# Performance work log

Hardware: AMD Instinct MI355X
Metric: run time of the kernel (lower is better)

## Reference

```python
import jax, jax.numpy as jnp
import numpy as np

HEADDIM = 128
CHUNK = 256


def _ssd_scan(x, dt, A, B, C, chunk):
    # x: (b,l,h,p)  dt: (b,l,h)  A: (h,)  B,C: (b,l,n)  (single group g=1 shared by all heads)
    b, l, h, p = x.shape
    n = B.shape[-1]
    nc = l // chunk
    dA = dt * A  # (b,l,h)
    xc = x.reshape(b, nc, chunk, h, p)
    dtc = dt.reshape(b, nc, chunk, h)
    dAc = dA.reshape(b, nc, chunk, h)
    Bc = B.reshape(b, nc, chunk, n)
    Cc = C.reshape(b, nc, chunk, n)
    cs = jnp.cumsum(dAc, axis=2)  # (b,nc,c,h) cumulative log-decay within chunk
    # intra-chunk quadratic part
    CB = jnp.einsum('bjin,bjkn->bjik', Cc, Bc)  # (b,nc,c,c)
    decay = jnp.exp(cs[:, :, :, None, :] - cs[:, :, None, :, :])  # (b,nc,i,k,h)
    mask = jnp.tril(jnp.ones((chunk, chunk), dtype=bool))
    decay = jnp.where(mask[None, None, :, :, None], decay, 0.0)
    y_intra = jnp.einsum('bjik,bjikh,bjkh,bjkhp->bjihp', CB, decay, dtc, xc)
    # per-chunk end states
    decay_states = jnp.exp(cs[:, :, -1:, :] - cs)  # (b,nc,c,h)
    states = jnp.einsum('bjkh,bjkh,bjkn,bjkhp->bjhnp', decay_states, dtc, Bc, xc)
    # recurrence across chunks: h_j = exp(sum dA_j) * h_{j-1} + states_j
    chunk_decay = jnp.exp(cs[:, :, -1, :])  # (b,nc,h)
    def step(carry, inp):
        s, d = inp
        new = carry * d[:, :, None, None] + s
        return new, carry  # emit state BEFORE this chunk
    init = jnp.zeros((b, h, n, p), x.dtype)
    _, prev = jax.lax.scan(step, init,
                           (states.transpose(1, 0, 2, 3, 4), chunk_decay.transpose(1, 0, 2)))
    prev = prev.transpose(1, 0, 2, 3, 4)  # (b,nc,h,n,p)
    y_inter = jnp.einsum('bjih,bjin,bjhnp->bjihp', jnp.exp(cs), Cc, prev)
    return (y_intra + y_inter).reshape(b, l, h, p)


def setup_inputs() -> dict:
    key = jax.random.key(0)
    k1, k2, k3, k4 = jax.random.split(key, 4)
    b, l, d_inner, nheads, d_state = 2, 4096, 2048, 16, 256
    x = jax.random.normal(k1, (b, l, d_inner), dtype=jnp.float32)
    BC = jax.random.normal(k2, (b, l, 2 * d_state), dtype=jnp.float32) * 0.1
    dt = jax.random.normal(k3, (b, l, 2 * nheads), dtype=jnp.float32) - 3.0
    A_log = jnp.zeros((nheads,), dtype=jnp.float32)
    D = jnp.ones((nheads,), dtype=jnp.float32)
    W_fcD = jax.random.normal(k4, (nheads, d_inner), dtype=jnp.float32) * 0.02
    return {"x": x, "BC": BC, "dt": dt, "A_log": A_log, "D": D, "W_fcD": W_fcD}


def reference(x, BC, dt, A_log, D, W_fcD):
    b, l, dim = x.shape
    h = A_log.shape[0]
    p = HEADDIM
    d_state = BC.shape[-1] // 2
    A = -jnp.exp(A_log)
    # bidirectional: concat forward stream with time-flipped backward stream along batch
    dt2 = jnp.concatenate((dt[:, :, :h], jnp.flip(dt[:, :, h:], axis=1)), axis=0)
    dt2 = jax.nn.softplus(dt2)
    x_og = x
    x2 = jnp.concatenate((x, jnp.flip(x, axis=1)), axis=0)
    BC2 = jnp.concatenate((BC, jnp.flip(BC, axis=1)), axis=0)
    B, C = BC2[..., :d_state], BC2[..., d_state:]
    y = _ssd_scan(x2.reshape(2 * b, l, h, p), dt2, A, B, C, CHUNK)
    y = y.reshape(2 * b, l, dim)
    y = jnp.roll(y, shift=1, axis=1).at[:, 0, :].set(0.0)
    y_fw, y_bw = y[:b], jnp.flip(y[b:], axis=1)
    gate = x_og @ W_fcD.T + D  # (b,l,h)
    y = y_fw + y_bw + x_og * jnp.repeat(gate, p, axis=-1)
    return y
```

## Files before the change

### kernel.cpp

```cpp
#include <hip/hip_runtime.h>
#include <stdint.h>

#define NB 2
#define SL 4096
#define NH 16
#define HD 128
#define DS 256
#define CK 256
#define NCH 16
#define NSQ 4
#define DI 2048

typedef unsigned short u16;
typedef unsigned int u32;
typedef __attribute__((ext_vector_type(8))) __bf16 bf16x8;
typedef __attribute__((ext_vector_type(4))) float f32x4;

__device__ __forceinline__ int tor(int dir, int t) { return dir ? (SL - 1 - t) : t; }

__device__ __forceinline__ u16 f2bf(float f) {
  u32 u = __float_as_uint(f);
  u = u + 0x7fffu + ((u >> 16) & 1u);
  return (u16)(u >> 16);
}
__device__ __forceinline__ float bf2f(u16 s) {
  return __uint_as_float(((u32)s) << 16);
}

__device__ __forceinline__ void gl_lds16(const u16* g, u16* l) {
  __builtin_amdgcn_global_load_lds((const __attribute__((address_space(1))) u32*)g,
                                   (__attribute__((address_space(3))) u32*)l, 16, 0, 0);
}

__device__ __forceinline__ void stage_tile(const u16* __restrict__ src, u16* lds,
                                           int lane, int w, int k0) {
  int sgrow = lane >> 2, sc = lane & 3;
  int r0 = w << 5;
  int ra = r0 + sgrow, rb = ra + 16;
  int kqa = (sc ^ ((ra >> 1) & 3)) << 3;
  int kqb = (sc ^ ((rb >> 1) & 3)) << 3;
  gl_lds16(src + (size_t)ra * 256 + k0 + kqa, lds + r0 * 32);
  gl_lds16(src + (size_t)rb * 256 + k0 + kqb, lds + (r0 + 16) * 32);
}

__device__ __forceinline__ bf16x8 frag(const u16* lds, int base_row, int m, int quad) {
  int row = base_row + m;
  return *(const bf16x8*)&lds[row * 32 + ((quad ^ ((row >> 1) & 3)) << 3)];
}

__device__ __forceinline__ void mfma16(const u16* As, const u16* Bs, int wi, int wp,
                                       int m, int quad, f32x4 acc[4][4]) {
  bf16x8 af[4], bv[4];
#pragma unroll
  for (int r = 0; r < 4; ++r) af[r] = frag(As, wi + (r << 4), m, quad);
#pragma unroll
  for (int c = 0; c < 4; ++c) bv[c] = frag(Bs, wp + (c << 4), m, quad);
#pragma unroll
  for (int r = 0; r < 4; ++r)
#pragma unroll
    for (int c = 0; c < 4; ++c)
      acc[r][c] = __builtin_amdgcn_mfma_f32_16x16x32_bf16(af[r], bv[c], acc[r][c], 0, 0, 0);
}

__global__ __launch_bounds__(256) void kprep(const float* __restrict__ dt,
                                             const float* __restrict__ A_log,
                                             float* __restrict__ csb,
                                             float* __restrict__ dtvb,
                                             float* __restrict__ cdecb) {
  int blk = blockIdx.x;
  int h = blk & 15, sj = blk >> 4;
  int s = sj >> 4, j = sj & 15;
  int b = s & 1, dir = s >> 1;
  int i = threadIdx.x;
  int to = tor(dir, j * CK + i);
  __shared__ float sbuf[CK];
  float a = -expf(A_log[h]);
  float raw = dt[((size_t)(b * SL + to)) * (2 * NH) + dir * NH + h];
  float sp = (raw > 20.f) ? raw : log1pf(expf(raw));
  sbuf[i] = sp * a;
  __syncthreads();
  for (int off = 1; off < CK; off <<= 1) {
    float v = (i >= off) ? sbuf[i - off] : 0.f;
    __syncthreads();
    sbuf[i] += v;
    __syncthreads();
  }
  float csv = sbuf[i];
  size_t base = ((size_t)sj * NH + h) * CK;
  csb[base + i] = csv;
  dtvb[base + i] = sp;
  if (i == CK - 1) cdecb[sj * NH + h] = expf(csv);
}

__global__ __launch_bounds__(256) void kcast(const float* __restrict__ BC,
                                             u16* __restrict__ Bbf,
                                             u16* __restrict__ Cbf) {
  int blk = blockIdx.x;
  int s = blk >> 12, t = blk & (SL - 1);
  int b = s & 1, dir = s >> 1;
  int tsrc = tor(dir, t);
  int tid = threadIdx.x;
  const float* src = BC + ((size_t)(b * SL + tsrc)) * (2 * DS);
  size_t dstb = ((size_t)s * SL + t) * DS;
  Bbf[dstb + tid] = f2bf(src[tid]);
  Cbf[dstb + tid] = f2bf(src[DS + tid]);
}

__global__ __launch_bounds__(256) void ktransB(const u16* __restrict__ Bbf,
                                               u16* __restrict__ BbfT) {
  int sj = blockIdx.x;
  int s = sj >> 4, j = sj & 15;
  __shared__ u16 T[64 * 264];
  int tid = threadIdx.x;
  const u16* src = Bbf + ((size_t)s * SL + j * CK) * DS;
  u16* dst = BbfT + (size_t)sj * DS * CK;
  int kr = tid >> 2, part = (tid & 3) * 64;
  for (int k0 = 0; k0 < CK; k0 += 64) {
    __syncthreads();
    {
      const uint4* gs = (const uint4*)(src + (size_t)(k0 + kr) * DS + part);
      uint4* tb = (uint4*)&T[kr * 264 + part];
#pragma unroll
      for (int q = 0; q < 8; ++q) tb[q] = gs[q];
    }
    __syncthreads();
    int n = tid;
    u16 col[64];
#pragma unroll
    for (int kq = 0; kq < 64; ++kq) col[kq] = T[kq * 264 + n];
    uint4* ds_ = (uint4*)(dst + (size_t)n * CK + k0);
#pragma unroll
    for (int q = 0; q < 8; ++q) {
      uint4 wv;
      wv.x = (u32)col[q * 8 + 0] | ((u32)col[q * 8 + 1] << 16);
      wv.y = (u32)col[q * 8 + 2] | ((u32)col[q * 8 + 3] << 16);
      wv.z = (u32)col[q * 8 + 4] | ((u32)col[q * 8 + 5] << 16);
      wv.w = (u32)col[q * 8 + 6] | ((u32)col[q * 8 + 7] << 16);
      ds_[q] = wv;
    }
  }
}

__global__ __launch_bounds__(256) void kxsT(const float* __restrict__ xg,
                                            const float* __restrict__ csb,
                                            const float* __restrict__ dtvb,
                                            u16* __restrict__ xsT) {
  int inst = blockIdx.x;
  int h = inst & 15, sj = inst >> 4;
  int s = sj >> 4, j = sj & 15;
  int b = s & 1, dir = s >> 1;
  int tid = threadIdx.x;
  __shared__ u16 Ls[128 * 40];
  size_t cbase = ((size_t)sj * NH + h) * CK;
  u16* dst = xsT + (size_t)inst * (128 * 256);
  int kk = tid >> 3;
  int pg = (tid & 7) * 16;
  int p2 = tid >> 1, half = tid & 1;
  for (int k0 = 0; k0 < CK; k0 += 32) {
    int kglob = k0 + kk;
    float sc_ = expf(-csb[cbase + kglob]) * dtvb[cbase + kglob];
    int t = tor(dir, j * CK + kglob);
    const float* src = xg + ((size_t)(b * SL + t)) * DI + h * HD + pg;
    float4 v0 = ((const float4*)src)[0];
    float4 v1 = ((const float4*)src)[1];
    float4 v2 = ((const float4*)src)[2];
    float4 v3 = ((const float4*)src)[3];
    float vv[16] = {v0.x, v0.y, v0.z, v0.w, v1.x, v1.y, v1.z, v1.w,
                    v2.x, v2.y, v2.z, v2.w, v3.x, v3.y, v3.z, v3.w};
    __syncthreads();
#pragma unroll
    for (int q = 0; q < 16; ++q) Ls[(pg + q) * 40 + kk] = f2bf(vv[q] * sc_);
    __syncthreads();
    uint4 w0 = *(const uint4*)&Ls[p2 * 40 + half * 16];
    uint4 w1 = *(const uint4*)&Ls[p2 * 40 + half * 16 + 8];
    *(uint4*)&dst[(size_t)p2 * 256 + k0 + half * 16] = w0;
    *(uint4*)&dst[(size_t)p2 * 256 + k0 + half * 16 + 8] = w1;
  }
}

__global__ __launch_bounds__(256) void kcb(const u16* __restrict__ Cbf,
                                           const u16* __restrict__ Bbf,
                                           u16* __restrict__ CBm) {
  int blk = blockIdx.x;
  int tri = blk % 3;
  int sj = blk / 3;
  int it0 = tri ? 128 : 0;
  int kt0 = (tri == 2) ? 128 : 0;
  int s = sj >> 4, j = sj & 15;
  __shared__ u16 As[128 * 32];
  __shared__ u16 Bs[128 * 32];
  int tid = threadIdx.x;
  int w = tid >> 6, lane = tid & 63;
  int wi = (w >> 1) << 6, wp = (w & 1) << 6;
  int m = lane & 15, quad = lane >> 4;
  const u16* Ab = Cbf + ((size_t)s * SL + j * CK + it0) * DS;
  const u16* Bb = Bbf + ((size_t)s * SL + j * CK + kt0) * DS;
  f32x4 zini = {0.f, 0.f, 0.f, 0.f};
  f32x4 acc[4][4];
#pragma unroll
  for (int r = 0; r < 4; ++r)
#pragma unroll
    for (int c = 0; c < 4; ++c) acc[r][c] = zini;
  for (int ks = 0; ks < 8; ++ks) {
    int k0 = ks << 5;
    stage_tile(Ab, As, lane, w, k0);
    stage_tile(Bb, Bs, lane, w, k0);
    __syncthreads();
    mfma16(As, Bs, wi, wp, m, quad, acc);
    __syncthreads();
  }
  int diag = (it0 == kt0);
  u16* dst = CBm + ((size_t)sj * CK + it0) * CK + kt0;
#pragma unroll
  for (int r = 0; r < 4; ++r)
#pragma unroll
    for (int rg = 0; rg < 4; ++rg) {
      int irow = wi + (r << 4) + (quad << 2) + rg;
#pragma unroll
      for (int c = 0; c < 4; ++c) {
        int kcol = wp + (c << 4) + m;
        float v = acc[r][c][rg];
        if (diag && kcol > irow) v = 0.f;
        dst[(size_t)irow * CK + kcol] = f2bf(v);
      }
    }
}

__global__ __launch_bounds__(256) void kstates(const u16* __restrict__ xsT,
                                               const u16* __restrict__ BbfT,
                                               const float* __restrict__ cdecb,
                                               u16* __restrict__ prevT) {
  int blk = blockIdx.x;
  int ntile = blk & 1;
  int inst = blk >> 1;
  int h = inst & 15, sj = inst >> 4;
  int nt0 = ntile << 7;
  __shared__ u16 As[128 * 32];
  __shared__ u16 Bs[128 * 32];
  int tid = threadIdx.x;
  int w = tid >> 6, lane = tid & 63;
  int wi = (w >> 1) << 6, wp = (w & 1) << 6;
  int m = lane & 15, quad = lane >> 4;
  const u16* Ab = xsT + (size_t)inst * (128 * 256);
  const u16* Bb = BbfT + ((size_t)sj * DS + nt0) * CK;
  f32x4 zini = {0.f, 0.f, 0.f, 0.f};
  f32x4 acc[4][4];
#pragma unroll
  for (int r = 0; r < 4; ++r)
#pragma unroll
    for (int c = 0; c < 4; ++c) acc[r][c] = zini;
  for (int ks = 0; ks < 8; ++ks) {
    int k0 = ks << 5;
    stage_tile(Ab, As, lane, w, k0);
    stage_tile(Bb, Bs, lane, w, k0);
    __syncthreads();
    mfma16(As, Bs, wi, wp, m, quad, acc);
    __syncthreads();
  }
  float scale = cdecb[sj * NH + h];
  u16* dst = prevT + (size_t)inst * (128 * 256) + nt0;
#pragma unroll
  for (int r = 0; r < 4; ++r)
#pragma unroll
    for (int rg = 0; rg < 4; ++rg) {
      int prow = wi + (r << 4) + (quad << 2) + rg;
#pragma unroll
      for (int c = 0; c < 4; ++c) {
        int ncol = wp + (c << 4) + m;
        dst[(size_t)prow * 256 + ncol] = f2bf(acc[r][c][rg] * scale);
      }
    }
}

__global__ __launch_bounds__(256) void kscan(u16* __restrict__ prevT,
                                             const float* __restrict__ cdecb) {
  int g = blockIdx.x * 256 + threadIdx.x;
  int n = g & 255;
  int p = (g >> 8) & 127;
  int h = (g >> 15) & 15;
  int s = g >> 19;
  size_t base = (((size_t)(s * 256 + h) * 128) + p) * 256 + n;
  const size_t stride = (size_t)NH * 128 * 256;
  float carry = 0.f;
  for (int j = 0; j < NCH; ++j) {
    size_t idx = base + (size_t)j * stride;
    float sv = bf2f(prevT[idx]);
    prevT[idx] = f2bf(carry);
    carry = carry * cdecb[(s * NCH + j) * NH + h] + sv;
  }
}

__global__ __launch_bounds__(256) void ky(const u16* __restrict__ CBm,
                                          const u16* __restrict__ Cbf,
                                          const u16* __restrict__ xsT,
                                          const u16* __restrict__ prevT,
                                          const float* __restrict__ csb,
                                          u16* __restrict__ ytmpb) {
  int blk = blockIdx.x;
  int itile = blk & 1;
  int inst = blk >> 1;
  int h = inst & 15, sj = inst >> 4;
  int s = sj >> 4, j = sj & 15;
  int it0 = itile << 7;
  __shared__ u16 As[128 * 32];
  __shared__ u16 Bs[128 * 32];
  int tid = threadIdx.x;
  int w = tid >> 6, lane = tid & 63;
  int wi = (w >> 1) << 6, wp = (w & 1) << 6;
  int m = lane & 15, quad = lane >> 4;

  const u16* Ai = CBm + ((size_t)sj * CK + it0) * CK;
  const u16* Ae = Cbf + ((size_t)s * SL + j * CK + it0) * DS;
  const u16* Bi = xsT + (size_t)inst * (128 * 256);
  const u16* Be = prevT + (size_t)inst * (128 * 256);

  int nIntra = itile ? 8 : 4;
  int nTot = nIntra + 8;

  f32x4 zini = {0.f, 0.f, 0.f, 0.f};
  f32x4 acc[4][4];
#pragma unroll
  for (int r = 0; r < 4; ++r)
#pragma unroll
    for (int c = 0; c < 4; ++c) acc[r][c] = zini;

  for (int ks = 0; ks < nTot; ++ks) {
    int intra = ks < nIntra;
    int k0 = (intra ? ks : ks - nIntra) << 5;
    const u16* Ab = intra ? Ai : Ae;
    const u16* Bb = intra ? Bi : Be;
    stage_tile(Ab, As, lane, w, k0);
    stage_tile(Bb, Bs, lane, w, k0);
    __syncthreads();
    mfma16(As, Bs, wi, wp, m, quad, acc);
    __syncthreads();
  }
  const float* csrow = csb + ((size_t)sj * NH + h) * CK + it0;
  u16* yb = ytmpb + ((size_t)s * SL + j * CK + it0) * DI + h * HD;
#pragma unroll
  for (int r = 0; r < 4; ++r)
#pragma unroll
    for (int rg = 0; rg < 4; ++rg) {
      int irow = wi + (r << 4) + (quad << 2) + rg;
      float esc = expf(csrow[irow]);
#pragma unroll
      for (int c = 0; c < 4; ++c) {
        int pcol = wp + (c << 4) + m;
        yb[(size_t)irow * DI + pcol] = f2bf(acc[r][c][rg] * esc);
      }
    }
}

__device__ __forceinline__ void unpk8(uint4 u, float* o) {
  o[0] = __uint_as_float(u.x << 16); o[1] = __uint_as_float(u.x & 0xffff0000u);
  o[2] = __uint_as_float(u.y << 16); o[3] = __uint_as_float(u.y & 0xffff0000u);
  o[4] = __uint_as_float(u.z << 16); o[5] = __uint_as_float(u.z & 0xffff0000u);
  o[6] = __uint_as_float(u.w << 16); o[7] = __uint_as_float(u.w & 0xffff0000u);
}

__global__ __launch_bounds__(256) void kfinal(const float* __restrict__ xg,
                                              const float* __restrict__ Wg,
                                              const float* __restrict__ Dg,
                                              const u16* __restrict__ ytmpb,
                                              float* __restrict__ out) {
  int bid = blockIdx.x;
  int b = bid >> 12;
  int t = bid & (SL - 1);
  __shared__ float xrow[DI];
  __shared__ float gp[4][NH];
  __shared__ float gate[NH];
  int tid = threadIdx.x;
  const float* xr = xg + ((size_t)(b * SL + t)) * DI;
  ((float4*)xrow)[tid] = ((const float4*)xr)[tid];
  ((float4*)xrow)[tid + 256] = ((const float4*)xr)[tid + 256];
  __syncthreads();
  float a[NH];
#pragma unroll
  for (int h = 0; h < NH; ++h) a[h] = 0.f;
#pragma unroll
  for (int q = 0; q < 8; ++q) {
    int d = q * 256 + tid;
    float xv = xrow[d];
#pragma unroll
    for (int h = 0; h < NH; ++h) a[h] += xv * Wg[h * DI + d];
  }
#pragma unroll
  for (int h = 0; h < NH; ++h) {
    float v = a[h];
    v += __shfl_down(v, 32);
    v += __shfl_down(v, 16);
    v += __shfl_down(v, 8);
    v += __shfl_down(v, 4);
    v += __shfl_down(v, 2);
    v += __shfl_down(v, 1);
    if ((tid & 63) == 0) gp[tid >> 6][h] = v;
  }
  __syncthreads();
  if (tid < NH) gate[tid] = gp[0][tid] + gp[1][tid] + gp[2][tid] + gp[3][tid] + Dg[tid];
  __syncthreads();
  int d0 = tid * 8;
  float g = gate[tid >> 4];
  float fy[8] = {0.f, 0.f, 0.f, 0.f, 0.f, 0.f, 0.f, 0.f};
  float by[8] = {0.f, 0.f, 0.f, 0.f, 0.f, 0.f, 0.f, 0.f};
  if (t > 0) {
    uint4 u = *(const uint4*)(ytmpb + ((size_t)(b * SL + (t - 1))) * DI + d0);
    unpk8(u, fy);
  }
  if (t < SL - 1) {
    uint4 u = *(const uint4*)(ytmpb + ((size_t)((2 + b) * SL + (SL - 2 - t))) * DI + d0);
    unpk8(u, by);
  }
  float* op = out + ((size_t)(b * SL + t)) * DI + d0;
#pragma unroll
  for (int q = 0; q < 8; ++q)
    op[q] = fy[q] + by[q] + xrow[d0 + q] * g;
}

extern "C" void kernel_launch(void* const* d_in, const int* in_sizes, int n_in,
                              void* d_out, int out_size, void* d_ws, size_t ws_size,
                              hipStream_t stream) {
  (void)in_sizes; (void)n_in; (void)out_size; (void)ws_size;
  const float* x     = (const float*)d_in[0];
  const float* BC    = (const float*)d_in[1];
  const float* dt    = (const float*)d_in[2];
  const float* A_log = (const float*)d_in[3];
  const float* Dg    = (const float*)d_in[4];
  const float* W     = (const float*)d_in[5];
  float* out = (float*)d_out;

  char* p = (char*)d_ws;
  float* cs   = (float*)p;  p += (size_t)NSQ * NCH * NH * CK * 4;
  float* dtv  = (float*)p;  p += (size_t)NSQ * NCH * NH * CK * 4;
  float* cdec = (float*)p;  p += (size_t)NSQ * NCH * NH * 4;
  u16* Bbf    = (u16*)p;    p += (size_t)NSQ * SL * DS * 2;
  u16* Cbf    = (u16*)p;    p += (size_t)NSQ * SL * DS * 2;
  u16* BbfT   = (u16*)p;    p += (size_t)NSQ * NCH * DS * CK * 2;
  u16* CBm    = (u16*)p;    p += (size_t)NSQ * NCH * CK * CK * 2;
  u16* xsT    = (u16*)p;    p += (size_t)NSQ * NCH * NH * HD * CK * 2;
  u16* prevT  = (u16*)p;    p += (size_t)NSQ * NCH * NH * HD * DS * 2;
  u16* ytmpb  = (u16*)p;    p += (size_t)NSQ * SL * DI * 2;

  hipLaunchKernelGGL(kprep,   dim3(NSQ * NCH * NH),      dim3(CK),  0, stream, dt, A_log, cs, dtv, cdec);
  hipLaunchKernelGGL(kcast,   dim3(NSQ * SL),            dim3(256), 0, stream, BC, Bbf, Cbf);
  hipLaunchKernelGGL(ktransB, dim3(NSQ * NCH),           dim3(256), 0, stream, Bbf, BbfT);
  hipLaunchKernelGGL(kxsT,    dim3(NSQ * NCH * NH),      dim3(256), 0, stream, x, cs, dtv, xsT);
  hipLaunchKernelGGL(kcb,     dim3(NSQ * NCH * 3),       dim3(256), 0, stream, Cbf, Bbf, CBm);
  hipLaunchKernelGGL(kstates, dim3(NSQ * NCH * NH * 2),  dim3(256), 0, stream, xsT, BbfT, cdec, prevT);
  hipLaunchKernelGGL(kscan,   dim3(NSQ * NH * HD * DS / 256), dim3(256), 0, stream, prevT, cdec);
  hipLaunchKernelGGL(ky,      dim3(NSQ * NCH * NH * 2),  dim3(256), 0, stream, CBm, Cbf, xsT, prevT, cs, ytmpb);
  hipLaunchKernelGGL(kfinal,  dim3(NB * SL),             dim3(256), 0, stream, x, W, Dg, ytmpb, out);
}
```

Before: 413.3 us.

## Tile final gate GEMV over 16 rows per block to reuse W

The final kernel now processes 16 time rows per block instead of one. The W_fcD weights are staged through shared memory in 256-column slices and reused across 4 rows per wavefront, which cuts the repeated global reads of W that each single-row block used to do. The output epilogue uses float4 stores and reads x directly from global memory instead of a shared-memory row. In exchange there are fewer blocks (512), higher register pressure from the 64 accumulators and 16 float4 weights, and x is read twice from global memory.

```diff
diff --git a/kernel.cpp b/kernel.cpp
--- a/kernel.cpp
+++ b/kernel.cpp
@@ -364,56 +364,90 @@
                                               const u16* __restrict__ ytmpb,
                                               float* __restrict__ out) {
   int bid = blockIdx.x;
-  int b = bid >> 12;
-  int t = bid & (SL - 1);
-  __shared__ float xrow[DI];
-  __shared__ float gp[4][NH];
-  __shared__ float gate[NH];
-  int tid = threadIdx.x;
-  const float* xr = xg + ((size_t)(b * SL + t)) * DI;
-  ((float4*)xrow)[tid] = ((const float4*)xr)[tid];
-  ((float4*)xrow)[tid + 256] = ((const float4*)xr)[tid + 256];
+  int b = bid >> 8;
+  int t0 = (bid & 255) << 4;
+  __shared__ float Wl[16 * 256];
+  __shared__ float gatel[16][16];
+  int tid = threadIdx.x;
+  int w = tid >> 6, lane = tid & 63;
+  int c4 = lane << 2;
+
+  float acc[4][16];
+#pragma unroll
+  for (int r = 0; r < 4; ++r)
+#pragma unroll
+    for (int h = 0; h < 16; ++h) acc[r][h] = 0.f;
+
+  for (int i = 0; i < 8; ++i) {
+    __syncthreads();
+#pragma unroll
+    for (int q = 0; q < 4; ++q) {
+      int idx = q * 256 + tid;
+      int h = idx >> 6;
+      int c = (idx & 63) << 2;
+      *(float4*)&Wl[h * 256 + c] = *(const float4*)&Wg[(size_t)h * DI + i * 256 + c];
+    }
+    __syncthreads();
+    float4 Wf[16];
+#pragma unroll
+    for (int h = 0; h < 16; ++h) Wf[h] = *(const float4*)&Wl[h * 256 + c4];
+#pragma unroll
+    for (int r = 0; r < 4; ++r) {
+      int t = t0 + (w << 2) + r;
+      float4 xv = *(const float4*)&xg[((size_t)(b * SL + t)) * DI + i * 256 + c4];
+#pragma unroll
+      for (int h = 0; h < 16; ++h)
+        acc[r][h] += xv.x * Wf[h].x + xv.y * Wf[h].y + xv.z * Wf[h].z + xv.w * Wf[h].w;
+    }
+  }
+#pragma unroll
+  for (int r = 0; r < 4; ++r)
+#pragma unroll
+    for (int h = 0; h < 16; ++h) {
+      float v = acc[r][h];
+      v += __shfl_xor(v, 32);
+      v += __shfl_xor(v, 16);
+      v += __shfl_xor(v, 8);
+      v += __shfl_xor(v, 4);
+      v += __shfl_xor(v, 2);
+      v += __shfl_xor(v, 1);
+      acc[r][h] = v;
+    }
+  if (lane == 0) {
+#pragma unroll
+    for (int r = 0; r < 4; ++r)
+#pragma unroll
+      for (int h = 0; h < 16; ++h) gatel[(w << 2) + r][h] = acc[r][h] + Dg[h];
+  }
   __syncthreads();
-  float a[NH];
-#pragma unroll
-  for (int h = 0; h < NH; ++h) a[h] = 0.f;
-#pragma unroll
-  for (int q = 0; q < 8; ++q) {
-    int d = q * 256 + tid;
-    float xv = xrow[d];
-#pragma unroll
-    for (int h = 0; h < NH; ++h) a[h] += xv * Wg[h * DI + d];
-  }
-#pragma unroll
-  for (int h = 0; h < NH; ++h) {
-    float v = a[h];
-    v += __shfl_down(v, 32);
-    v += __shfl_down(v, 16);
-    v += __shfl_down(v, 8);
-    v += __shfl_down(v, 4);
-    v += __shfl_down(v, 2);
-    v += __shfl_down(v, 1);
-    if ((tid & 63) == 0) gp[tid >> 6][h] = v;
-  }
-  __syncthreads();
-  if (tid < NH) gate[tid] = gp[0][tid] + gp[1][tid] + gp[2][tid] + gp[3][tid] + Dg[tid];
-  __syncthreads();
-  int d0 = tid * 8;
-  float g = gate[tid >> 4];
-  float fy[8] = {0.f, 0.f, 0.f, 0.f, 0.f, 0.f, 0.f, 0.f};
-  float by[8] = {0.f, 0.f, 0.f, 0.f, 0.f, 0.f, 0.f, 0.f};
-  if (t > 0) {
-    uint4 u = *(const uint4*)(ytmpb + ((size_t)(b * SL + (t - 1))) * DI + d0);
-    unpk8(u, fy);
-  }
-  if (t < SL - 1) {
-    uint4 u = *(const uint4*)(ytmpb + ((size_t)((2 + b) * SL + (SL - 2 - t))) * DI + d0);
-    unpk8(u, by);
-  }
-  float* op = out + ((size_t)(b * SL + t)) * DI + d0;
-#pragma unroll
-  for (int q = 0; q < 8; ++q)
-    op[q] = fy[q] + by[q] + xrow[d0 + q] * g;
+
+  int d0 = tid << 3;
+  int h8 = tid >> 4;
+  const u16* fwbase = ytmpb + (size_t)b * SL * DI + d0;
+  const u16* bwbase = ytmpb + (size_t)(2 + b) * SL * DI + d0;
+#pragma unroll 2
+  for (int r = 0; r < 16; ++r) {
+    int t = t0 + r;
+    size_t rowb = ((size_t)(b * SL + t)) * DI + d0;
+    float4 x0 = *(const float4*)&xg[rowb];
+    float4 x1 = *(const float4*)&xg[rowb + 4];
+    float fy[8] = {0.f, 0.f, 0.f, 0.f, 0.f, 0.f, 0.f, 0.f};
+    float by[8] = {0.f, 0.f, 0.f, 0.f, 0.f, 0.f, 0.f, 0.f};
+    if (t > 0) unpk8(*(const uint4*)(fwbase + (size_t)(t - 1) * DI), fy);
+    if (t < SL - 1) unpk8(*(const uint4*)(bwbase + (size_t)(SL - 2 - t) * DI), by);
+    float g = gatel[r][h8];
+    float4 o0, o1;
+    o0.x = fy[0] + by[0] + x0.x * g;
+    o0.y = fy[1] + by[1] + x0.y * g;
+    o0.z = fy[2] + by[2] + x0.z * g;
+    o0.w = fy[3] + by[3] + x0.w * g;
+    o1.x = fy[4] + by[4] + x1.x * g;
+    o1.y = fy[5] + by[5] + x1.y * g;
+    o1.z = fy[6] + by[6] + x1.z * g;
+    o1.w = fy[7] + by[7] + x1.w * g;
+    *(float4*)&out[rowb] = o0;
+    *(float4*)&out[rowb + 4] = o1;
+  }
 }
 
 extern "C" void kernel_launch(void* const* d_in, const int* in_sizes, int n_in,
@@ -448,5 +482,5 @@
   hipLaunchKernelGGL(kstates, dim3(NSQ * NCH * NH * 2),  dim3(256), 0, stream, xsT, BbfT, cdec, prevT);
   hipLaunchKernelGGL(kscan,   dim3(NSQ * NH * HD * DS / 256), dim3(256), 0, stream, prevT, cdec);
   hipLaunchKernelGGL(ky,      dim3(NSQ * NCH * NH * 2),  dim3(256), 0, stream, CBm, Cbf, xsT, prevT, cs, ytmpb);
-  hipLaunchKernelGGL(kfinal,  dim3(NB * SL),             dim3(256), 0, stream, x, W, Dg, ytmpb, out);
-}
+  hipLaunchKernelGGL(kfinal,  dim3(NB * SL / 16),        dim3(256), 0, stream, x, W, Dg, ytmpb, out);
+}
```

Result: faster. 387.2 us (-6.3%).
